# Optimization experiments

Measured on AMD Instinct MI355X. Metric: run time of the kernel, lower is better.

The kernel has to match this reference:

```python
import jax, jax.numpy as jnp
import numpy as np

D_MODEL = 1024
HEADS = 16
HEAD_DIM = D_MODEL // HEADS
SEQ_LEN = 2048
BATCH = 2
LN_EPS = 1e-5


def _layernorm(x, gamma, beta):
    mu = jnp.mean(x, axis=-1, keepdims=True)
    var = jnp.var(x, axis=-1, keepdims=True)
    return (x - mu) * jax.lax.rsqrt(var + LN_EPS) * gamma + beta


def setup_inputs() -> dict:
    key = jax.random.key(0)
    ks = jax.random.split(key, 12)
    d, h = D_MODEL, 4 * D_MODEL
    s = lambda fan_in: 1.0 / np.sqrt(fan_in)
    return {
        "x": jax.random.normal(ks[0], (BATCH, SEQ_LEN, d), dtype=jnp.float32),
        "W_qkv": jax.random.uniform(ks[1], (d, 3 * d), minval=-s(d), maxval=s(d)),
        "b_qkv": jax.random.uniform(ks[2], (3 * d,), minval=-s(d), maxval=s(d)),
        "W1": jax.random.uniform(ks[3], (d, h), minval=-s(d), maxval=s(d)),
        "b1": jax.random.uniform(ks[4], (h,), minval=-s(d), maxval=s(d)),
        "W2": jax.random.uniform(ks[5], (h, d), minval=-s(h), maxval=s(h)),
        "b2": jax.random.uniform(ks[6], (d,), minval=-s(h), maxval=s(h)),
        "ln1_g": jnp.ones((d,), jnp.float32),
        "ln1_b": jnp.zeros((d,), jnp.float32),
        "ln2_g": jnp.ones((d,), jnp.float32),
        "ln2_b": jnp.zeros((d,), jnp.float32),
    }


def reference(x, W_qkv, b_qkv, W1, b1, W2, b2, ln1_g, ln1_b, ln2_g, ln2_b):
    B, T, C = x.shape
    # QKV projection -> [B, T, 3, H, hs] -> q,k,v each [B, H, T, hs]
    qkv = (x @ W_qkv + b_qkv).reshape(B, T, 3, HEADS, HEAD_DIM)
    qkv = jnp.transpose(qkv, (2, 0, 3, 1, 4))
    q, k, v = qkv[0], qkv[1], qkv[2]
    # Naive causal attention with full [B,H,T,T] score matrix (matches source)
    A = jnp.einsum("bhqd,bhkd->bhqk", q, k) / jnp.sqrt(jnp.float32(HEAD_DIM))
    causal = jnp.tril(jnp.ones((T, T), dtype=bool))
    A = jnp.where(causal, A, -jnp.inf)
    A = jax.nn.softmax(A, axis=-1)
    attn = jnp.einsum("bhqk,bhkd->bhqd", A, v)  # [B,H,T,hs]
    attn = jnp.transpose(attn, (0, 2, 1, 3)).reshape(B, T, C)
    # Residual + LN, FFN, residual + LN (dropout=0 / eval)
    h = _layernorm(x + attn, ln1_g, ln1_b)
    ff = jax.nn.relu(h @ W1 + b1) @ W2 + b2
    return _layernorm(h + ff, ln2_g, ln2_b)
```

## Files before the change

### kernel.cpp

```cpp
#include <hip/hip_runtime.h>

#define D_MODEL 1024
#define HEADS   16
#define HEAD_DIM 64
#define SEQ     2048
#define BATCH   2
#define ROWS    (BATCH*SEQ)
#define FFDIM   4096

typedef __attribute__((ext_vector_type(8))) short short8;
typedef __attribute__((ext_vector_type(4))) float f32x4;
typedef __attribute__((ext_vector_type(4))) unsigned short us4;

typedef const __attribute__((address_space(1))) unsigned int* gptr_t;
typedef __attribute__((address_space(3))) unsigned int* lptr_t;

__device__ __forceinline__ unsigned short f2bf(float f){
  unsigned int x = __float_as_uint(f);
  x += 0x7fffu + ((x >> 16) & 1u);
  return (unsigned short)(x >> 16);
}

__device__ __forceinline__ float wave_sum(float x){
  #pragma unroll
  for (int off = 32; off; off >>= 1) x += __shfl_xor(x, off);
  return x;
}

__global__ __launch_bounds__(256) void cast_bf16_kernel(const float* __restrict__ in,
                                                        unsigned short* __restrict__ out, int n4){
  int i = blockIdx.x * 256 + threadIdx.x;
  if (i >= n4) return;
  float4 v = *(const float4*)(in + (size_t)i * 4);
  us4 o;
  o[0] = f2bf(v.x); o[1] = f2bf(v.y); o[2] = f2bf(v.z); o[3] = f2bf(v.w);
  *(us4*)(out + (size_t)i * 4) = o;
}

__global__ __launch_bounds__(256) void transpose_cast_kernel(const float* __restrict__ in,
                                                             unsigned short* __restrict__ out,
                                                             int R, int C){
  __shared__ float tile[32][33];
  const int bc = blockIdx.x * 32, br = blockIdx.y * 32;
  const int tx = threadIdx.x & 31, ty = threadIdx.x >> 5;
  #pragma unroll
  for (int j = 0; j < 4; ++j)
    tile[ty + 8*j][tx] = in[(size_t)(br + ty + 8*j) * C + bc + tx];
  __syncthreads();
  #pragma unroll
  for (int j = 0; j < 4; ++j)
    out[(size_t)(bc + ty + 8*j) * R + br + tx] = f2bf(tile[tx][ty + 8*j]);
}

template<int EPI>
__global__ __launch_bounds__(256) void gemm_kernel(const unsigned short* __restrict__ A,
                                                   const unsigned short* __restrict__ BT,
                                                   const float* __restrict__ bias,
                                                   int M, int N, int K, int kchunk,
                                                   int gx, int gy,
                                                   float* __restrict__ outF,
                                                   unsigned short* __restrict__ outH,
                                                   unsigned short* __restrict__ qo,
                                                   unsigned short* __restrict__ ko,
                                                   unsigned short* __restrict__ vT){
  __shared__ __align__(16) unsigned short Alds[2][128 * 32];
  __shared__ __align__(16) unsigned short Blds[2][128 * 32];
  const int tid = threadIdx.x;
  const int lane = tid & 63;
  const int wid = tid >> 6;
  const int wr = wid >> 1, wc = wid & 1;
  const int lrow = lane & 15, lgrp = lane >> 4;

  const int nwg = gridDim.x;
  const int cpx = nwg >> 3;
  const int wg = (blockIdx.x & 7) * cpx + (blockIdx.x >> 3);
  const int nx = wg % gx;
  const int rest = wg / gx;
  const int my = rest % gy;
  const int sk = rest / gy;

  const int m0 = my * 128, n0 = nx * 128;
  const int kbase0 = sk * kchunk;

  const int sr = lane >> 2, sc = (lane & 3) * 8;

  f32x4 acc[4][4];
  #pragma unroll
  for (int i = 0; i < 4; ++i)
    #pragma unroll
    for (int j = 0; j < 4; ++j)
      acc[i][j] = f32x4{0.f, 0.f, 0.f, 0.f};

  #pragma unroll
  for (int it = 0; it < 2; ++it){
    const int c = wid * 2 + it;
    const int r = c * 16 + sr;
    __builtin_amdgcn_global_load_lds(
        (gptr_t)(const void*)(A + (size_t)(m0 + r) * K + kbase0 + sc),
        (lptr_t)(void*)(&Alds[0][c * 512]), 16, 0, 0);
    __builtin_amdgcn_global_load_lds(
        (gptr_t)(const void*)(BT + (size_t)(n0 + r) * K + kbase0 + sc),
        (lptr_t)(void*)(&Blds[0][c * 512]), 16, 0, 0);
  }

  const int nk = kchunk >> 5;
  int cur = 0;
  for (int kt = 0; kt < nk; ++kt){
    __syncthreads();

    if (kt + 1 < nk){
      const int kb = kbase0 + (kt + 1) * 32;
      #pragma unroll
      for (int it = 0; it < 2; ++it){
        const int c = wid * 2 + it;
        const int r = c * 16 + sr;
        __builtin_amdgcn_global_load_lds(
            (gptr_t)(const void*)(A + (size_t)(m0 + r) * K + kb + sc),
            (lptr_t)(void*)(&Alds[cur ^ 1][c * 512]), 16, 0, 0);
        __builtin_amdgcn_global_load_lds(
            (gptr_t)(const void*)(BT + (size_t)(n0 + r) * K + kb + sc),
            (lptr_t)(void*)(&Blds[cur ^ 1][c * 512]), 16, 0, 0);
      }
    }

    short8 af[4], bfr[4];
    #pragma unroll
    for (int f = 0; f < 4; ++f){
      af[f]  = *(const short8*)&Alds[cur][(wr * 64 + f * 16 + lrow) * 32 + lgrp * 8];
      bfr[f] = *(const short8*)&Blds[cur][(wc * 64 + f * 16 + lrow) * 32 + lgrp * 8];
    }
    __builtin_amdgcn_s_setprio(1);
    #pragma unroll
    for (int i = 0; i < 4; ++i)
      #pragma unroll
      for (int j = 0; j < 4; ++j)
        acc[i][j] = __builtin_amdgcn_mfma_f32_16x16x32_bf16(af[i], bfr[j], acc[i][j], 0, 0, 0);
    __builtin_amdgcn_s_setprio(0);
    cur ^= 1;
  }

  float* const outP = (EPI == 3) ? outF + (size_t)sk * M * N : outF;
  #pragma unroll
  for (int i = 0; i < 4; ++i){
    const int rg = m0 + wr * 64 + i * 16 + lgrp * 4;
    #pragma unroll
    for (int j = 0; j < 4; ++j){
      const int cg = n0 + wc * 64 + j * 16 + lrow;
      const float bb = (EPI == 3) ? 0.f : bias[cg];
      if constexpr (EPI == 0){
        const int which = cg >> 10, rem = cg & 1023;
        const int hh = rem >> 6, dd = rem & 63;
        const int bb_ = rg >> 11, tt = rg & 2047;
        const size_t bh = (size_t)(bb_ * HEADS + hh);
        if (which == 2){
          us4 pk;
          #pragma unroll
          for (int r = 0; r < 4; ++r) pk[r] = f2bf(acc[i][j][r] + bb);
          *(us4*)(vT + (bh * 64 + dd) * SEQ + tt) = pk;
        } else {
          unsigned short* dst = which ? ko : qo;
          const float sc2 = which ? 1.0f : 0.125f;
          #pragma unroll
          for (int r = 0; r < 4; ++r)
            dst[(bh * SEQ + tt + r) * 64 + dd] = f2bf((acc[i][j][r] + bb) * sc2);
        }
      } else if constexpr (EPI == 1){
        #pragma unroll
        for (int r = 0; r < 4; ++r)
          outH[(size_t)(rg + r) * N + cg] = f2bf(fmaxf(acc[i][j][r] + bb, 0.f));
      } else {
        #pragma unroll
        for (int r = 0; r < 4; ++r)
          outP[(size_t)(rg + r) * N + cg] = acc[i][j][r] + bb;
      }
    }
  }
}

__global__ __launch_bounds__(256) void attn_mfma_kernel(const unsigned short* __restrict__ Qb,
                                                        const unsigned short* __restrict__ Kb,
                                                        const unsigned short* __restrict__ VT,
                                                        float* __restrict__ Op){
  __shared__ __align__(16) char Kl[2][8192];
  __shared__ __align__(16) char Vl[2][8192];
  __shared__ __align__(16) char Pl[4][4096];
  const int tid = threadIdx.x;
  const int w = tid >> 6, lane = tid & 63;
  const int lr = lane & 15, g = lane >> 4;

  const int bx = blockIdx.x, u = bx & 255, half = bx >> 8;
  const int g8 = u >> 5;
  const int qg = half ? g8 : 15 - g8;
  const int bh = u & 31;

  const int q0w = qg * 128 + w * 32;
  const int qA = q0w + lr, qB = qA + 16;

  const char* const KbB = (const char*)(Kb + (size_t)bh * SEQ * 64);
  const char* const VbB = (const char*)(VT + (size_t)bh * 64 * SEQ);
  char* const PbA = Pl[w];
  char* const PbB = Pl[w] + 2048;

  const unsigned short* qra = Qb + ((size_t)bh * SEQ + qA) * 64 + g * 8;
  const short8 qfA0 = *(const short8*)(qra);
  const short8 qfA1 = *(const short8*)(qra + 32);
  const short8 qfB0 = *(const short8*)(qra + 16 * 64);
  const short8 qfB1 = *(const short8*)(qra + 16 * 64 + 32);

  f32x4 oA[4], oB[4];
  #pragma unroll
  for (int dt = 0; dt < 4; ++dt){ oA[dt] = f32x4{0.f,0.f,0.f,0.f}; oB[dt] = f32x4{0.f,0.f,0.f,0.f}; }
  float mA = -INFINITY, lA = 0.f, mB = -INFINITY, lB = 0.f;
  const int swzl = (lr & 7) << 4;

  const int kbmax = 2 * qg + 1;

  short8 st[4];
  {
    #pragma unroll
    for (int c = 0; c < 2; ++c){
      const int L = c * 4096 + tid * 16;
      st[c] = *(const short8*)(KbB + L);
      const int row = L >> 7, col = L & 127;
      st[2 + c] = *(const short8*)(VbB + (size_t)row * 4096 + col);
    }
  }

  for (int kb = 0; kb <= kbmax; ++kb){
    const int p = kb & 1;
    const int k0 = kb * 64;

    #pragma unroll
    for (int c = 0; c < 2; ++c){
      const int L = c * 4096 + tid * 16;
      const int row = L >> 7, col = L & 127;
      const int dst = row * 128 + (col ^ ((row & 7) << 4));
      *(short8*)(Kl[p] + dst) = st[c];
      *(short8*)(Vl[p] + dst) = st[2 + c];
    }
    __syncthreads();

    if (kb < kbmax){
      #pragma unroll
      for (int c = 0; c < 2; ++c){
        const int L = c * 4096 + tid * 16;
        st[c] = *(const short8*)(KbB + (size_t)(kb + 1) * 8192 + L);
        const int row = L >> 7, col = L & 127;
        st[2 + c] = *(const short8*)(VbB + (size_t)row * 4096 + (size_t)(kb + 1) * 128 + col);
      }
    }

    f32x4 sA[4], sB[4];
    __builtin_amdgcn_s_setprio(1);
    #pragma unroll
    for (int kt = 0; kt < 4; ++kt){
      const int row = kt * 16 + lr;
      const int ro = row * 128, sw = (row & 7) << 4;
      const short8 kf0 = *(const short8*)(Kl[p] + ro + ((g * 16) ^ sw));
      const short8 kf1 = *(const short8*)(Kl[p] + ro + ((64 + g * 16) ^ sw));
      sA[kt] = __builtin_amdgcn_mfma_f32_16x16x32_bf16(kf0, qfA0, f32x4{0.f,0.f,0.f,0.f}, 0, 0, 0);
      sA[kt] = __builtin_amdgcn_mfma_f32_16x16x32_bf16(kf1, qfA1, sA[kt], 0, 0, 0);
      sB[kt] = __builtin_amdgcn_mfma_f32_16x16x32_bf16(kf0, qfB0, f32x4{0.f,0.f,0.f,0.f}, 0, 0, 0);
      sB[kt] = __builtin_amdgcn_mfma_f32_16x16x32_bf16(kf1, qfB1, sB[kt], 0, 0, 0);
    }
    __builtin_amdgcn_s_setprio(0);

    if (kb >= kbmax - 1){
      #pragma unroll
      for (int kt = 0; kt < 4; ++kt)
        #pragma unroll
        for (int r = 0; r < 4; ++r){
          const int key = k0 + kt * 16 + g * 4 + r;
          if (key > qA) sA[kt][r] = -INFINITY;
          if (key > qB) sB[kt][r] = -INFINITY;
        }
    }

    {
      float mx = -INFINITY;
      #pragma unroll
      for (int kt = 0; kt < 4; ++kt)
        #pragma unroll
        for (int r = 0; r < 4; ++r) mx = fmaxf(mx, sA[kt][r]);
      mx = fmaxf(mx, __shfl_xor(mx, 16));
      mx = fmaxf(mx, __shfl_xor(mx, 32));
      const float mn = fmaxf(mA, mx);
      const float corr = __expf(mA - mn);
      float sum = 0.f;
      #pragma unroll
      for (int kt = 0; kt < 4; ++kt)
        #pragma unroll
        for (int r = 0; r < 4; ++r){
          const float pp = __expf(sA[kt][r] - mn);
          sA[kt][r] = pp; sum += pp;
        }
      sum += __shfl_xor(sum, 16);
      sum += __shfl_xor(sum, 32);
      lA = lA * corr + sum; mA = mn;
      #pragma unroll
      for (int kt = 0; kt < 4; ++kt){
        us4 pk;
        #pragma unroll
        for (int r = 0; r < 4; ++r) pk[r] = f2bf(sA[kt][r]);
        *(us4*)(PbA + lr * 128 + ((kt * 32 + g * 8) ^ swzl)) = pk;
      }
      float oc[4];
      #pragma unroll
      for (int r = 0; r < 4; ++r) oc[r] = __shfl(corr, g * 4 + r);
      #pragma unroll
      for (int dt = 0; dt < 4; ++dt)
        #pragma unroll
        for (int r = 0; r < 4; ++r) oA[dt][r] *= oc[r];
    }
    {
      float mx = -INFINITY;
      #pragma unroll
      for (int kt = 0; kt < 4; ++kt)
        #pragma unroll
        for (int r = 0; r < 4; ++r) mx = fmaxf(mx, sB[kt][r]);
      mx = fmaxf(mx, __shfl_xor(mx, 16));
      mx = fmaxf(mx, __shfl_xor(mx, 32));
      const float mn = fmaxf(mB, mx);
      const float corr = __expf(mB - mn);
      float sum = 0.f;
      #pragma unroll
      for (int kt = 0; kt < 4; ++kt)
        #pragma unroll
        for (int r = 0; r < 4; ++r){
          const float pp = __expf(sB[kt][r] - mn);
          sB[kt][r] = pp; sum += pp;
        }
      sum += __shfl_xor(sum, 16);
      sum += __shfl_xor(sum, 32);
      lB = lB * corr + sum; mB = mn;
      #pragma unroll
      for (int kt = 0; kt < 4; ++kt){
        us4 pk;
        #pragma unroll
        for (int r = 0; r < 4; ++r) pk[r] = f2bf(sB[kt][r]);
        *(us4*)(PbB + lr * 128 + ((kt * 32 + g * 8) ^ swzl)) = pk;
      }
      float oc[4];
      #pragma unroll
      for (int r = 0; r < 4; ++r) oc[r] = __shfl(corr, g * 4 + r);
      #pragma unroll
      for (int dt = 0; dt < 4; ++dt)
        #pragma unroll
        for (int r = 0; r < 4; ++r) oB[dt][r] *= oc[r];
    }

    const short8 paA0 = *(const short8*)(PbA + lr * 128 + ((g * 16) ^ swzl));
    const short8 paA1 = *(const short8*)(PbA + lr * 128 + ((64 + g * 16) ^ swzl));
    const short8 paB0 = *(const short8*)(PbB + lr * 128 + ((g * 16) ^ swzl));
    const short8 paB1 = *(const short8*)(PbB + lr * 128 + ((64 + g * 16) ^ swzl));
    __builtin_amdgcn_s_setprio(1);
    #pragma unroll
    for (int dt = 0; dt < 4; ++dt){
      const int row = dt * 16 + lr;
      const int ro = row * 128, sw = (row & 7) << 4;
      const short8 vf0 = *(const short8*)(Vl[p] + ro + ((g * 16) ^ sw));
      const short8 vf1 = *(const short8*)(Vl[p] + ro + ((64 + g * 16) ^ sw));
      oA[dt] = __builtin_amdgcn_mfma_f32_16x16x32_bf16(paA0, vf0, oA[dt], 0, 0, 0);
      oA[dt] = __builtin_amdgcn_mfma_f32_16x16x32_bf16(paA1, vf1, oA[dt], 0, 0, 0);
      oB[dt] = __builtin_amdgcn_mfma_f32_16x16x32_bf16(paB0, vf0, oB[dt], 0, 0, 0);
      oB[dt] = __builtin_amdgcn_mfma_f32_16x16x32_bf16(paB1, vf1, oB[dt], 0, 0, 0);
    }
    __builtin_amdgcn_s_setprio(0);
  }

  const int b = bh >> 4, hh = bh & 15;
  {
    float lv[4];
    #pragma unroll
    for (int r = 0; r < 4; ++r) lv[r] = __shfl(lA, g * 4 + r);
    #pragma unroll
    for (int dt = 0; dt < 4; ++dt)
      #pragma unroll
      for (int r = 0; r < 4; ++r)
        Op[((size_t)(b * SEQ) + q0w + g * 4 + r) * D_MODEL + hh * 64 + dt * 16 + lr] = oA[dt][r] / lv[r];
  }
  {
    float lv[4];
    #pragma unroll
    for (int r = 0; r < 4; ++r) lv[r] = __shfl(lB, g * 4 + r);
    #pragma unroll
    for (int dt = 0; dt < 4; ++dt)
      #pragma unroll
      for (int r = 0; r < 4; ++r)
        Op[((size_t)(b * SEQ) + q0w + 16 + g * 4 + r) * D_MODEL + hh * 64 + dt * 16 + lr] = oB[dt][r] / lv[r];
  }
}

__global__ __launch_bounds__(256) void ln_kernel(const float* __restrict__ A,
                                                 const float* __restrict__ B1,
                                                 const float* __restrict__ B2,
                                                 const float* __restrict__ bias,
                                                 const float* __restrict__ g,
                                                 const float* __restrict__ be,
                                                 float* __restrict__ outF,
                                                 unsigned short* __restrict__ outH){
  const int row = blockIdx.x, tid = threadIdx.x;
  const size_t base = (size_t)row * D_MODEL + tid * 4;
  float4 va = *(const float4*)(A + base);
  float4 vb = *(const float4*)(B1 + base);
  float v0 = va.x + vb.x, v1 = va.y + vb.y, v2 = va.z + vb.z, v3 = va.w + vb.w;
  if (B2){
    float4 vc = *(const float4*)(B2 + base);
    v0 += vc.x; v1 += vc.y; v2 += vc.z; v3 += vc.w;
  }
  if (bias){
    float4 vd = *(const float4*)(bias + tid * 4);
    v0 += vd.x; v1 += vd.y; v2 += vd.z; v3 += vd.w;
  }
  float s  = v0 + v1 + v2 + v3;
  float ss = v0*v0 + v1*v1 + v2*v2 + v3*v3;
  s = wave_sum(s); ss = wave_sum(ss);
  __shared__ float red[8];
  const int w = tid >> 6, lane = tid & 63;
  if (!lane){ red[w] = s; red[4 + w] = ss; }
  __syncthreads();
  s  = red[0] + red[1] + red[2] + red[3];
  ss = red[4] + red[5] + red[6] + red[7];
  const float mu  = s * (1.0f / D_MODEL);
  const float var = ss * (1.0f / D_MODEL) - mu * mu;
  const float rstd = rsqrtf(var + 1e-5f);
  float4 gg = *(const float4*)(g  + tid * 4);
  float4 bb = *(const float4*)(be + tid * 4);
  const float r0 = (v0 - mu) * rstd * gg.x + bb.x;
  const float r1 = (v1 - mu) * rstd * gg.y + bb.y;
  const float r2 = (v2 - mu) * rstd * gg.z + bb.z;
  const float r3 = (v3 - mu) * rstd * gg.w + bb.w;
  float4 of; of.x = r0; of.y = r1; of.z = r2; of.w = r3;
  *(float4*)(outF + base) = of;
  if (outH){
    us4 oh; oh[0] = f2bf(r0); oh[1] = f2bf(r1); oh[2] = f2bf(r2); oh[3] = f2bf(r3);
    *(us4*)(outH + base) = oh;
  }
}

extern "C" void kernel_launch(void* const* d_in, const int* in_sizes, int n_in,
                              void* d_out, int out_size, void* d_ws, size_t ws_size,
                              hipStream_t stream){
  (void)in_sizes; (void)n_in; (void)out_size;
  const float* x     = (const float*)d_in[0];
  const float* W_qkv = (const float*)d_in[1];
  const float* b_qkv = (const float*)d_in[2];
  const float* W1    = (const float*)d_in[3];
  const float* b1    = (const float*)d_in[4];
  const float* W2    = (const float*)d_in[5];
  const float* b2    = (const float*)d_in[6];
  const float* ln1g  = (const float*)d_in[7];
  const float* ln1b  = (const float*)d_in[8];
  const float* ln2g  = (const float*)d_in[9];
  const float* ln2b  = (const float*)d_in[10];

  char* ws = (char*)d_ws;
  const size_t MB = 1024ull * 1024ull;
  unsigned short* WqkvT = (unsigned short*)(ws + 0 * MB);
  unsigned short* W1T   = (unsigned short*)(ws + 6 * MB);
  unsigned short* W2T   = (unsigned short*)(ws + 14 * MB);
  unsigned short* xbf   = (unsigned short*)(ws + 22 * MB);
  unsigned short* qB    = (unsigned short*)(ws + 30 * MB);
  unsigned short* kB    = (unsigned short*)(ws + 39 * MB);
  unsigned short* vT    = (unsigned short*)(ws + 48 * MB);
  float* attn = (float*)(ws + 57 * MB);
  float* hF           = (float*)(ws + 30 * MB);
  unsigned short* hB  = (unsigned short*)(ws + 46 * MB);
  unsigned short* ff1 = (unsigned short*)(ws + 54 * MB);
  float* p0           = (float*)(ws + 86 * MB);
  float* p1           = (float*)(ws + 102 * MB);

  const int nsplit = (ws_size >= 119 * MB) ? 2 : 1;

  cast_bf16_kernel<<<4096, 256, 0, stream>>>(x, xbf, ROWS * D_MODEL / 4);
  transpose_cast_kernel<<<dim3(96, 32), 256, 0, stream>>>(W_qkv, WqkvT, 1024, 3072);
  transpose_cast_kernel<<<dim3(128, 32), 256, 0, stream>>>(W1, W1T, 1024, 4096);
  transpose_cast_kernel<<<dim3(32, 128), 256, 0, stream>>>(W2, W2T, 4096, 1024);

  gemm_kernel<0><<<768, 256, 0, stream>>>(
      xbf, WqkvT, b_qkv, ROWS, 3072, 1024, 1024, 24, 32, nullptr, nullptr, qB, kB, vT);

  attn_mfma_kernel<<<512, 256, 0, stream>>>(qB, kB, vT, attn);

  ln_kernel<<<ROWS, 256, 0, stream>>>(x, attn, nullptr, nullptr, ln1g, ln1b, hF, hB);

  gemm_kernel<1><<<1024, 256, 0, stream>>>(
      hB, W1T, b1, ROWS, FFDIM, 1024, 1024, 32, 32, nullptr, ff1, nullptr, nullptr, nullptr);

  gemm_kernel<3><<<256 * nsplit, 256, 0, stream>>>(
      ff1, W2T, nullptr, ROWS, 1024, FFDIM, FFDIM / nsplit, 8, 32, p0, nullptr, nullptr, nullptr, nullptr);

  ln_kernel<<<ROWS, 256, 0, stream>>>(hF, p0, (nsplit == 2) ? p1 : nullptr, b2,
                                      ln2g, ln2b, (float*)d_out, nullptr);
}
```

Before: 239.8 us.

## Deepen GEMM LDS pipeline to four stages and group M-tiles for L2 reuse

The GEMM main loop moves from double-buffered LDS to a 4-slot ring with three tiles prefetched ahead. Explicit vmcnt waits and a raw s_barrier replace the per-iteration __syncthreads, so global-to-LDS loads have more time to complete before use. The workgroup-to-tile mapping now groups four consecutive M tiles per N column, which should improve L2 reuse of B. LDS use doubles to 64KB, which may lower occupancy, and the mapping assumes gy is divisible by 4.

```diff
diff --git a/kernel.cpp b/kernel.cpp
--- a/kernel.cpp
+++ b/kernel.cpp
@@ -63,8 +63,8 @@
                                                    unsigned short* __restrict__ qo,
                                                    unsigned short* __restrict__ ko,
                                                    unsigned short* __restrict__ vT){
-  __shared__ __align__(16) unsigned short Alds[2][128 * 32];
-  __shared__ __align__(16) unsigned short Blds[2][128 * 32];
+  __shared__ __align__(16) unsigned short Alds[4][128 * 32];
+  __shared__ __align__(16) unsigned short Blds[4][128 * 32];
   const int tid = threadIdx.x;
   const int lane = tid & 63;
   const int wid = tid >> 6;
@@ -74,10 +74,13 @@
   const int nwg = gridDim.x;
   const int cpx = nwg >> 3;
   const int wg = (blockIdx.x & 7) * cpx + (blockIdx.x >> 3);
-  const int nx = wg % gx;
-  const int rest = wg / gx;
-  const int my = rest % gy;
-  const int sk = rest / gy;
+  const int inb = wg & 3;
+  const int rest1 = wg >> 2;
+  const int nx = rest1 % gx;
+  const int rest2 = rest1 / gx;
+  const int gy4 = gy >> 2;
+  const int my = (rest2 % gy4) * 4 + inb;
+  const int sk = rest2 / gy4;
 
   const int m0 = my * 128, n0 = nx * 128;
   const int kbase0 = sk * kchunk;
@@ -91,43 +94,42 @@
     for (int j = 0; j < 4; ++j)
       acc[i][j] = f32x4{0.f, 0.f, 0.f, 0.f};
 
-  #pragma unroll
-  for (int it = 0; it < 2; ++it){
-    const int c = wid * 2 + it;
-    const int r = c * 16 + sr;
-    __builtin_amdgcn_global_load_lds(
-        (gptr_t)(const void*)(A + (size_t)(m0 + r) * K + kbase0 + sc),
-        (lptr_t)(void*)(&Alds[0][c * 512]), 16, 0, 0);
-    __builtin_amdgcn_global_load_lds(
-        (gptr_t)(const void*)(BT + (size_t)(n0 + r) * K + kbase0 + sc),
-        (lptr_t)(void*)(&Blds[0][c * 512]), 16, 0, 0);
-  }
-
   const int nk = kchunk >> 5;
-  int cur = 0;
-  for (int kt = 0; kt < nk; ++kt){
-    __syncthreads();
-
-    if (kt + 1 < nk){
-      const int kb = kbase0 + (kt + 1) * 32;
-      #pragma unroll
-      for (int it = 0; it < 2; ++it){
-        const int c = wid * 2 + it;
-        const int r = c * 16 + sr;
-        __builtin_amdgcn_global_load_lds(
-            (gptr_t)(const void*)(A + (size_t)(m0 + r) * K + kb + sc),
-            (lptr_t)(void*)(&Alds[cur ^ 1][c * 512]), 16, 0, 0);
-        __builtin_amdgcn_global_load_lds(
-            (gptr_t)(const void*)(BT + (size_t)(n0 + r) * K + kb + sc),
-            (lptr_t)(void*)(&Blds[cur ^ 1][c * 512]), 16, 0, 0);
-      }
-    }
+
+  auto STAGE = [&](int t, int slot){
+    const int kb = kbase0 + t * 32;
+    #pragma unroll
+    for (int it = 0; it < 2; ++it){
+      const int c = wid * 2 + it;
+      const int r = c * 16 + sr;
+      __builtin_amdgcn_global_load_lds(
+          (gptr_t)(const void*)(A + (size_t)(m0 + r) * K + kb + sc),
+          (lptr_t)(void*)(&Alds[slot][c * 512]), 16, 0, 0);
+      __builtin_amdgcn_global_load_lds(
+          (gptr_t)(const void*)(BT + (size_t)(n0 + r) * K + kb + sc),
+          (lptr_t)(void*)(&Blds[slot][c * 512]), 16, 0, 0);
+    }
+  };
+
+  STAGE(0, 0);
+  if (nk > 1) STAGE(1, 1);
+  if (nk > 2) STAGE(2, 2);
+
+  for (int t = 0; t < nk; ++t){
+    const int slot = t & 3;
+    if (t + 2 < nk)      asm volatile("s_waitcnt vmcnt(8)" ::: "memory");
+    else if (t + 1 < nk) asm volatile("s_waitcnt vmcnt(4)" ::: "memory");
+    else                 asm volatile("s_waitcnt vmcnt(0)" ::: "memory");
+    __builtin_amdgcn_s_barrier();
+    __builtin_amdgcn_sched_barrier(0);
+
+    if (t + 3 < nk) STAGE(t + 3, (t + 3) & 3);
 
     short8 af[4], bfr[4];
     #pragma unroll
     for (int f = 0; f < 4; ++f){
-      af[f]  = *(const short8*)&Alds[cur][(wr * 64 + f * 16 + lrow) * 32 + lgrp * 8];
-      bfr[f] = *(const short8*)&Blds[cur][(wc * 64 + f * 16 + lrow) * 32 + lgrp * 8];
+      af[f]  = *(const short8*)&Alds[slot][(wr * 64 + f * 16 + lrow) * 32 + lgrp * 8];
+      bfr[f] = *(const short8*)&Blds[slot][(wc * 64 + f * 16 + lrow) * 32 + lgrp * 8];
     }
     __builtin_amdgcn_s_setprio(1);
     #pragma unroll
@@ -136,7 +138,6 @@
       for (int j = 0; j < 4; ++j)
         acc[i][j] = __builtin_amdgcn_mfma_f32_16x16x32_bf16(af[i], bfr[j], acc[i][j], 0, 0, 0);
     __builtin_amdgcn_s_setprio(0);
-    cur ^= 1;
   }
 
   float* const outP = (EPI == 3) ? outF + (size_t)sk * M * N : outF;
```

New measurement: 253.9 us. +5.9%, slower.

## Add 256x256-tile, 512-thread GEMM kernel for the FFN up-projection

Applied to the files above, without the earlier changes.

Adds a dedicated GEMM kernel for the W1 projection. It uses 256x256 output tiles with 8 waves, each wave computing a 128x64 sub-tile, and double-buffers global-to-LDS loads with an XOR swizzle. It also remaps blocks into XCD-aware groups. Larger tiles raise arithmetic intensity and operand reuse per LDS load. The cost is more accumulator registers per thread (128 floats), only 256 blocks, and a single LDS sync per k-step, so occupancy or latency hiding may suffer.

```diff
diff --git a/kernel.cpp b/kernel.cpp
--- a/kernel.cpp
+++ b/kernel.cpp
@@ -173,6 +173,89 @@
         for (int r = 0; r < 4; ++r)
           outP[(size_t)(rg + r) * N + cg] = acc[i][j][r] + bb;
       }
+    }
+  }
+}
+
+__global__ __launch_bounds__(512, 2) void gemm256_kernel(const unsigned short* __restrict__ A,
+                                                         const unsigned short* __restrict__ BT,
+                                                         const float* __restrict__ bias,
+                                                         int M, int N, int K, int gx,
+                                                         unsigned short* __restrict__ outH){
+  __shared__ __align__(16) unsigned short Al[2][256 * 32];
+  __shared__ __align__(16) unsigned short Bl[2][256 * 32];
+  const int tid = threadIdx.x;
+  const int lane = tid & 63;
+  const int wid = tid >> 6;
+  const int wm = wid >> 2, wn = wid & 3;
+  const int lr = lane & 15, g = lane >> 4;
+
+  const int nwg = gridDim.x;
+  const int cpx = nwg >> 3;
+  const int wg = (blockIdx.x & 7) * cpx + (blockIdx.x >> 3);
+  const int nx = wg % gx, my = wg / gx;
+  const int m0 = my * 256, n0 = nx * 256;
+
+  f32x4 acc[8][4];
+  #pragma unroll
+  for (int i = 0; i < 8; ++i)
+    #pragma unroll
+    for (int j = 0; j < 4; ++j)
+      acc[i][j] = f32x4{0.f, 0.f, 0.f, 0.f};
+
+  auto STAGE = [&](int buf, int kt){
+    const int kb = kt * 32;
+    #pragma unroll
+    for (int j = 0; j < 2; ++j){
+      const int cc = tid + j * 512;
+      const int row = cc >> 2, c = cc & 3;
+      const int scol = ((c ^ (row & 3)) << 3);
+      __builtin_amdgcn_global_load_lds(
+          (gptr_t)(const void*)(A + (size_t)(m0 + row) * K + kb + scol),
+          (lptr_t)(void*)(&Al[buf][cc * 8]), 16, 0, 0);
+      __builtin_amdgcn_global_load_lds(
+          (gptr_t)(const void*)(BT + (size_t)(n0 + row) * K + kb + scol),
+          (lptr_t)(void*)(&Bl[buf][cc * 8]), 16, 0, 0);
+    }
+  };
+
+  const int nk = K >> 5;
+  STAGE(0, 0);
+  for (int t = 0; t < nk; ++t){
+    const int buf = t & 1;
+    __syncthreads();
+    if (t + 1 < nk) STAGE(buf ^ 1, t + 1);
+
+    short8 af[8], bf[4];
+    #pragma unroll
+    for (int i = 0; i < 8; ++i){
+      const int row = wm * 128 + i * 16 + lr;
+      af[i] = *(const short8*)&Al[buf][row * 32 + ((g * 8) ^ ((row & 3) << 3))];
+    }
+    #pragma unroll
+    for (int j = 0; j < 4; ++j){
+      const int row = wn * 64 + j * 16 + lr;
+      bf[j] = *(const short8*)&Bl[buf][row * 32 + ((g * 8) ^ ((row & 3) << 3))];
+    }
+    __builtin_amdgcn_s_setprio(1);
+    #pragma unroll
+    for (int i = 0; i < 8; ++i)
+      #pragma unroll
+      for (int j = 0; j < 4; ++j)
+        acc[i][j] = __builtin_amdgcn_mfma_f32_16x16x32_bf16(af[i], bf[j], acc[i][j], 0, 0, 0);
+    __builtin_amdgcn_s_setprio(0);
+  }
+
+  #pragma unroll
+  for (int i = 0; i < 8; ++i){
+    const int rg = m0 + wm * 128 + i * 16 + g * 4;
+    #pragma unroll
+    for (int j = 0; j < 4; ++j){
+      const int cg = n0 + wn * 64 + j * 16 + lr;
+      const float bb = bias[cg];
+      #pragma unroll
+      for (int r = 0; r < 4; ++r)
+        outH[(size_t)(rg + r) * N + cg] = f2bf(fmaxf(acc[i][j][r] + bb, 0.f));
     }
   }
 }
@@ -484,8 +567,8 @@
 
   ln_kernel<<<ROWS, 256, 0, stream>>>(x, attn, nullptr, nullptr, ln1g, ln1b, hF, hB);
 
-  gemm_kernel<1><<<1024, 256, 0, stream>>>(
-      hB, W1T, b1, ROWS, FFDIM, 1024, 1024, 32, 32, nullptr, ff1, nullptr, nullptr, nullptr);
+  gemm256_kernel<<<256, 512, 0, stream>>>(
+      hB, W1T, b1, ROWS, FFDIM, 1024, 16, ff1);
 
   gemm_kernel<3><<<256 * nsplit, 256, 0, stream>>>(
       ff1, W2T, nullptr, ROWS, 1024, FFDIM, FFDIM / nsplit, 8, 32, p0, nullptr, nullptr, nullptr, nullptr);
```

Measured after the change: 231.2 us. 3.6% less time.
